# Kernel optimization log

Hardware: AMD Instinct MI355X
Metric: run time of the kernel (lower is better)

## Reference

```python
import jax, jax.numpy as jnp
import numpy as np

# sizes
N, B, NPG = 8192, 8, 1024          # total nodes, graphs, nodes per graph (equal-size graphs)
D, H, DH, L = 256, 8, 32, 2        # hidden, heads, head dim, layers
IN_C, OUT_D, E, DFF = 128, 64, 262144, 512
EPS = 1e-5


def setup_inputs() -> dict:
    key = jax.random.key(0)
    ks = jax.random.split(key, 20)
    p = lambda i, shp: jax.random.normal(ks[i], shp, jnp.float32) * 0.05
    return dict(
        x=jax.random.normal(ks[0], (N, IN_C), jnp.float32),
        edge_index=jax.random.randint(ks[1], (2, E), 0, N),
        batch=jnp.arange(N, dtype=jnp.int32) // NPG,  # sorted, equal-size graphs
        w_in=p(2, (D, IN_C)), b_in=p(3, (D,)),
        sage_wl=p(4, (L, D, D)), sage_bl=p(5, (L, D)), sage_wr=p(6, (L, D, D)),
        attn_iw=p(7, (L, 3 * D, D)), attn_ib=p(8, (L, 3 * D)),
        attn_ow=p(9, (L, D, D)), attn_ob=p(10, (L, D)),
        n1_w=jnp.ones((L, D)), n1_b=jnp.zeros((L, D)),
        n2_w=jnp.ones((L, D)), n2_b=jnp.zeros((L, D)),
        n3_w=jnp.ones((L, D)), n3_b=jnp.zeros((L, D)),
        mlp_w1=p(11, (L, DFF, D)), mlp_b1=p(12, (L, DFF)),
        mlp_w2=p(13, (L, D, DFF)), mlp_b2=p(14, (L, D)),
        bn_w=jnp.ones((L, D)), bn_b=jnp.zeros((L, D)),
        w_out=p(15, (OUT_D, D)), b_out=p(16, (OUT_D,)),
    )


def _bn(h, w, b):
    # BatchNorm1d over nodes (training-mode batch statistics, biased var)
    m = h.mean(0)
    v = jnp.mean((h - m) ** 2, axis=0)
    return (h - m) * jax.lax.rsqrt(v + EPS) * w + b


def _forward(x, edge_index, batch, w_in, b_in, sage_wl, sage_bl, sage_wr,
             attn_iw, attn_ib, attn_ow, attn_ob, n1_w, n1_b, n2_w, n2_b,
             n3_w, n3_b, mlp_w1, mlp_b1, mlp_w2, mlp_b2, bn_w, bn_b, w_out, b_out):
    src, dst = edge_index[0], edge_index[1]
    deg = jax.ops.segment_sum(jnp.ones((E,), jnp.float32), dst, num_segments=N)
    inv_deg = (1.0 / jnp.clip(deg, 1.0))[:, None]
    scale = 1.0 / np.sqrt(DH)

    h = x @ w_in.T + b_in  # in_proj Linear  [N, D]
    for l in range(L):
        # --- GPSConv: local SAGEConv (mean aggr) + residual + norm1 ---
        agg = jax.ops.segment_sum(h[src], dst, num_segments=N) * inv_deg
        loc = agg @ sage_wl[l].T + sage_bl[l] + h @ sage_wr[l].T
        loc = _bn(loc + h, n1_w[l], n1_b[l])
        # --- GPSConv: dense per-graph multi-head self-attention + residual + norm2 ---
        hd = h.reshape(B, NPG, D)  # to_dense_batch (no padding: equal graph sizes)
        qkv = hd @ attn_iw[l].T + attn_ib[l]  # [B, n, 3D]
        q, k, v = jnp.split(qkv, 3, axis=-1)
        sh = lambda t: t.reshape(B, NPG, H, DH).transpose(0, 2, 1, 3)  # [B, H, n, DH]
        a = jax.nn.softmax(jnp.einsum('bhqd,bhkd->bhqk', sh(q) * scale, sh(k)), axis=-1)
        o = jnp.einsum('bhqk,bhkd->bhqd', a, sh(v)).transpose(0, 2, 1, 3).reshape(B, NPG, D)
        o = (o @ attn_ow[l].T + attn_ob[l]).reshape(N, D)
        glob = _bn(o + h, n2_w[l], n2_b[l])
        # --- GPSConv: sum branches, MLP residual, norm3 ---
        out = loc + glob
        out = out + jax.nn.relu(out @ mlp_w1[l].T + mlp_b1[l]) @ mlp_w2[l].T + mlp_b2[l]
        out = _bn(out, n3_w[l], n3_b[l])
        # --- outer GPS: BatchNorm + relu + (dropout=eval) + residual ---
        h = h + jax.nn.relu(_bn(out, bn_w[l], bn_b[l]))
    pooled = h.reshape(B, NPG, D).mean(axis=1)  # global_mean_pool over sorted equal-size graphs
    return pooled @ w_out.T + b_out  # [B, OUT_D]


def reference(x, edge_index, batch, w_in, b_in, sage_wl, sage_bl, sage_wr,
              attn_iw, attn_ib, attn_ow, attn_ob, n1_w, n1_b, n2_w, n2_b,
              n3_w, n3_b, mlp_w1, mlp_b1, mlp_w2, mlp_b2, bn_w, bn_b, w_out, b_out):
    return _forward(x, edge_index, batch, w_in, b_in, sage_wl, sage_bl, sage_wr,
                    attn_iw, attn_ib, attn_ow, attn_ob, n1_w, n1_b, n2_w, n2_b,
                    n3_w, n3_b, mlp_w1, mlp_b1, mlp_w2, mlp_b2, bn_w, bn_b, w_out, b_out)
```

## Files before the change

### kernel.cpp

```cpp
#include <hip/hip_runtime.h>
#include <hip/hip_bf16.h>

#define N_NODES 8192
#define BGRAPH 8
#define NPG 1024
#define DIM 256
#define NH 8
#define DHEAD 32
#define NLAYERS 2
#define INC 128
#define OUTD 64
#define NEDGE 262144
#define DFF 512
#define EPS 1e-5f

typedef __attribute__((ext_vector_type(4))) float f32x4;
typedef __attribute__((ext_vector_type(8))) short s16x8;
typedef __attribute__((ext_vector_type(4))) ushort u16x4;

__device__ __forceinline__ float b2f(ushort u){
  unsigned v = ((unsigned)u) << 16;
  return __builtin_bit_cast(float, v);
}
__device__ __forceinline__ ushort f2b(float f){
  unsigned u = __builtin_bit_cast(unsigned, f);
  u += 0x7fffu + ((u >> 16) & 1u);
  return (ushort)(u >> 16);
}
__device__ __forceinline__ ushort f2b_trunc(float f){
  return (ushort)(__builtin_bit_cast(unsigned, f) >> 16);
}
__device__ __forceinline__ void gload16(const void* g, void* l){
  __builtin_amdgcn_global_load_lds(
    (const __attribute__((address_space(1))) void*)g,
    (__attribute__((address_space(3))) void*)l,
    16, 0, 0);
}

#define CX  1048576
#define CWI (CX+32768)
#define CSW (CWI+262144)
#define CIW (CSW+393216)
#define COW (CIW+131072)
#define CW1 (COW+262144)
#define CW2 (CW1+262144)
#define NCAST (CW2/256)
__global__ void k_setup(const float* __restrict__ x, const float* __restrict__ w_in,
    const float* __restrict__ wl, const float* __restrict__ wr,
    const float* __restrict__ iw, const float* __restrict__ ow,
    const float* __restrict__ w1, const float* __restrict__ w2,
    ushort* __restrict__ dst, const int* __restrict__ edst, int* __restrict__ deg){
  if(blockIdx.x >= NCAST){
    int i = (blockIdx.x - NCAST)*256 + threadIdx.x;
    int stride = 512*256;
    for(; i<NEDGE; i+=stride) atomicAdd(&deg[edst[i]], 1);
    return;
  }
  int i = blockIdx.x*256 + threadIdx.x;
  float val;
  if(i < CX)       val = x[i];
  else if(i < CWI) val = w_in[i-CX];
  else if(i < CSW){
    int j = i - CWI;
    int l = j >> 17, r = (j >> 9) & 255, k = j & 511;
    val = (k < 256) ? wl[(l<<16) + (r<<8) + k] : wr[(l<<16) + (r<<8) + (k-256)];
  }
  else if(i < CIW) val = iw[i-CSW];
  else if(i < COW) val = ow[i-CIW];
  else if(i < CW1) val = w1[i-COW];
  else             val = w2[i-CW1];
  dst[i] = f2b(val);
}

__global__ void k_scan(const int* __restrict__ deg, int* __restrict__ offs,
                       float* __restrict__ inv_deg){
  __shared__ int s[1024];
  int t = threadIdx.x;
  int base = t*8;
  int loc[8]; int acc=0;
  #pragma unroll
  for(int j=0;j<8;j++){
    int dv = deg[base+j];
    inv_deg[base+j] = 1.0f/(float)(dv>0?dv:1);
    loc[j]=acc; acc += dv;
  }
  s[t]=acc;
  __syncthreads();
  for(int d=1; d<1024; d<<=1){
    int v = (t>=d)? s[t-d] : 0;
    __syncthreads();
    if(t>=d) s[t]+=v;
    __syncthreads();
  }
  int pre = (t>0)? s[t-1] : 0;
  #pragma unroll
  for(int j=0;j<8;j++) offs[base+j] = pre + loc[j];
  if(t==1023) offs[N_NODES] = s[1023];
}

#define STAGE_AB(t, buf) do{ \
    int kt_ = (t)*64; \
    _Pragma("unroll") \
    for(int it=0; it<2; ++it){ \
      int c = (wave*2+it)*64 + lane; \
      int row = c >> 3, q = c & 7; \
      int qs = q ^ (row & 7); \
      gload16(A + (size_t)(bm+row)*lda + kt_ + qs*8, (char*)As + (buf)*8192 + (wave*2+it)*1024); \
      gload16(W + (size_t)(bn+row)*K   + kt_ + qs*8, (char*)Bs + (buf)*8192 + (wave*2+it)*1024); \
    } \
  }while(0)

#define MM_COMPUTE(BUFOFF) \
      _Pragma("unroll") \
      for(int kk=0; kk<2; ++kk){ \
        s16x8 af[2], bfr[2]; \
        _Pragma("unroll") \
        for(int mi=0; mi<2; ++mi){ \
          int row = wr*32 + mi*16 + l15; \
          int col = (kk*64 + l4*16) ^ ((row & 7) << 4); \
          af[mi] = *(const s16x8*)((const char*)As + (BUFOFF) + row*128 + col); \
        } \
        _Pragma("unroll") \
        for(int nj=0; nj<2; ++nj){ \
          int row = wc*32 + nj*16 + l15; \
          int col = (kk*64 + l4*16) ^ ((row & 7) << 4); \
          bfr[nj] = *(const s16x8*)((const char*)Bs + (BUFOFF) + row*128 + col); \
        } \
        _Pragma("unroll") \
        for(int mi=0; mi<2; ++mi) \
          _Pragma("unroll") \
          for(int nj=0; nj<2; ++nj) \
            acc[mi][nj] = __builtin_amdgcn_mfma_f32_16x16x32_bf16(af[mi], bfr[nj], acc[mi][nj], 0,0,0); \
      }

#define MM_LOOP \
  f32x4 acc[2][2] = {}; \
  { const int nt = K >> 6; \
    STAGE_AB(0, 0); \
    asm volatile("s_waitcnt vmcnt(0)" ::: "memory"); \
    __builtin_amdgcn_s_barrier(); \
    int cur = 0; \
    for(int t=0; t<nt; ++t){ \
      if(t+1 < nt) STAGE_AB(t+1, cur^1); \
      MM_COMPUTE(cur*8192) \
      asm volatile("s_waitcnt vmcnt(0)" ::: "memory"); \
      __builtin_amdgcn_s_barrier(); \
      cur ^= 1; \
    } \
  }

#define MM_LOOP_SB \
  f32x4 acc[2][2] = {}; \
  { const int nt = K >> 6; \
    for(int t=0; t<nt; ++t){ \
      __syncthreads(); \
      STAGE_AB(t, 0); \
      asm volatile("s_waitcnt vmcnt(0)" ::: "memory"); \
      __builtin_amdgcn_s_barrier(); \
      MM_COMPUTE(0) \
    } \
  }

template<bool RELU, bool RESIDB, bool BIAS, bool WBF, bool STATS>
__global__ __launch_bounds__(256) void k_mm(const ushort* __restrict__ A,
    const ushort* __restrict__ W, const float* __restrict__ bias,
    const ushort* __restrict__ residb, ushort* __restrict__ Cb,
    float* __restrict__ gS, float* __restrict__ gQ,
    int M, int Nc, int K, int lda, int ldcb, int ldrb)
{
  __shared__ ushort As[2*64*64];
  __shared__ ushort Bs[2*64*64];
  __shared__ float sredS[64];
  __shared__ float sredQ[64];
  const int tid = threadIdx.x;
  const int lane = tid & 63, wave = tid >> 6;
  const int l15 = lane & 15, l4 = lane >> 4;
  const int bm = blockIdx.y*64, bn = blockIdx.x*64;
  const int wr = wave >> 1, wc = wave & 1;
  MM_LOOP

  float sloc[2] = {0.f,0.f}, qloc[2] = {0.f,0.f};
  #pragma unroll
  for(int mi=0; mi<2; ++mi){
    #pragma unroll
    for(int nj=0; nj<2; ++nj){
      int col = bn + wc*32 + nj*16 + l15;
      float bv = BIAS ? bias[col] : 0.f;
      #pragma unroll
      for(int r=0; r<4; ++r){
        int row = bm + wr*32 + mi*16 + l4*4 + r;
        float v = acc[mi][nj][r] + bv;
        if(RESIDB) v += b2f(residb[(size_t)row*ldrb + col]);
        if(RELU)   v = fmaxf(v, 0.f);
        if(WBF)    Cb[(size_t)row*ldcb + col] = f2b(v);
        if(STATS){ sloc[nj] += v; qloc[nj] += v*v; }
      }
    }
  }
  if(STATS){
    if(tid < 64){ sredS[tid]=0.f; sredQ[tid]=0.f; }
    __syncthreads();
    int c0 = wc*32 + l15;
    atomicAdd(&sredS[c0],    sloc[0]); atomicAdd(&sredQ[c0],    qloc[0]);
    atomicAdd(&sredS[c0+16], sloc[1]); atomicAdd(&sredQ[c0+16], qloc[1]);
    __syncthreads();
    if(tid < 64){
      atomicAdd(&gS[bn+tid], sredS[tid]);
      atomicAdd(&gQ[bn+tid], sredQ[tid]);
    }
  }
}

__global__ __launch_bounds__(256) void k_fill_inproj(const int* __restrict__ src,
    const int* __restrict__ dst, const int* __restrict__ offs,
    int* __restrict__ cursor, int* __restrict__ csr,
    const ushort* __restrict__ xb, const ushort* __restrict__ w_in_b,
    const float* __restrict__ b_in, ushort* __restrict__ hwb)
{
  __shared__ __align__(16) char smem[16384];
  const int tid = threadIdx.x;
  if(blockIdx.x < 512){
    int i = blockIdx.x*256 + tid;
    for(; i<NEDGE; i+=512*256){
      int d = dst[i];
      int p = atomicAdd(&cursor[d], 1);
      csr[offs[d]+p] = src[i];
    }
  } else {
    int idx = blockIdx.x - 512;
    const int lane = tid & 63, wave = tid >> 6;
    const int l15 = lane & 15, l4 = lane >> 4;
    const int bn = (idx & 3)*64, bm = (idx >> 2)*64;
    const int wr = wave >> 1, wc = wave & 1;
    const ushort* A = xb;
    const ushort* W = w_in_b;
    const int K = INC, lda = INC;
    ushort* As = (ushort*)smem;
    ushort* Bs = As + 4096;
    MM_LOOP_SB
    #pragma unroll
    for(int mi=0; mi<2; ++mi){
      #pragma unroll
      for(int nj=0; nj<2; ++nj){
        int col = bn + wc*32 + nj*16 + l15;
        float bv = b_in[col];
        #pragma unroll
        for(int r=0; r<4; ++r){
          int row = bm + wr*32 + mi*16 + l4*4 + r;
          hwb[(size_t)row*512 + 256 + col] = f2b(acc[mi][nj][r] + bv);
        }
      }
    }
  }
}

__global__ __launch_bounds__(256) void k_agg_qkv(ushort* __restrict__ hwb,
    const int* __restrict__ offs, const int* __restrict__ csr,
    const float* __restrict__ inv_deg, const ushort* __restrict__ iwb,
    const float* __restrict__ attn_ib, ushort* __restrict__ qpack,
    ushort* __restrict__ kpack, ushort* __restrict__ vpack)
{
  __shared__ __align__(16) char smem[16384];
  const int tid = threadIdx.x;
  const int lane = tid & 63, wave = tid >> 6;
  if(blockIdx.x < 2048){
    int n = blockIdx.x*4 + wave;
    int beg = offs[n], end = offs[n+1];
    f32x4 a0 = {0,0,0,0}, a1 = {0,0,0,0}, a2 = {0,0,0,0}, a3 = {0,0,0,0};
    int i = beg;
    for(; i+4<=end; i+=4){
      int j0=csr[i], j1=csr[i+1], j2=csr[i+2], j3=csr[i+3];
      u16x4 v0 = *(const u16x4*)(hwb + (size_t)j0*512 + 256 + lane*4);
      u16x4 v1 = *(const u16x4*)(hwb + (size_t)j1*512 + 256 + lane*4);
      u16x4 v2 = *(const u16x4*)(hwb + (size_t)j2*512 + 256 + lane*4);
      u16x4 v3 = *(const u16x4*)(hwb + (size_t)j3*512 + 256 + lane*4);
      #pragma unroll
      for(int c=0;c<4;c++){ a0[c]+=b2f(v0[c]); a1[c]+=b2f(v1[c]);
                            a2[c]+=b2f(v2[c]); a3[c]+=b2f(v3[c]); }
    }
    for(; i<end; ++i){
      int j0=csr[i];
      u16x4 v0 = *(const u16x4*)(hwb + (size_t)j0*512 + 256 + lane*4);
      #pragma unroll
      for(int c=0;c<4;c++) a0[c]+=b2f(v0[c]);
    }
    float inv = inv_deg[n];
    u16x4 outv;
    #pragma unroll
    for(int c=0;c<4;c++) outv[c] = f2b((a0[c]+a1[c]+a2[c]+a3[c])*inv);
    *(u16x4*)(hwb + (size_t)n*512 + lane*4) = outv;
  } else {
    int idx = blockIdx.x - 2048;
    const int bn = (idx % 12)*64, bm = (idx / 12)*64;
    const int l15 = lane & 15, l4 = lane >> 4;
    const int wr = wave >> 1, wc = wave & 1;
    const ushort* A = hwb + 256;
    const ushort* W = iwb;
    const int K = 256, lda = 512;
    ushort* As = (ushort*)smem;
    ushort* Bs = As + 4096;
    MM_LOOP_SB
    const int bgq = bm >> 10;
    #pragma unroll
    for(int mi=0; mi<2; ++mi){
      #pragma unroll
      for(int nj=0; nj<2; ++nj){
        int col = bn + wc*32 + nj*16 + l15;
        float bv = attn_ib[col];
        int part = col >> 8;
        int hh = (col >> 5) & 7;
        int dd = col & 31;
        ushort* dstp = (part==0 ? qpack : (part==1 ? kpack : vpack))
                     + (size_t)(bgq*8 + hh)*32768 + dd;
        #pragma unroll
        for(int r=0; r<4; ++r){
          int rig = (bm + wr*32 + mi*16 + l4*4 + r) & 1023;
          dstp[rig*32] = f2b(acc[mi][nj][r] + bv);
        }
      }
    }
  }
}

__global__ __launch_bounds__(256) void k_attn_sage(const ushort* __restrict__ qpack,
    const ushort* __restrict__ kpack, const ushort* __restrict__ vpack,
    ushort* __restrict__ attnO, const ushort* __restrict__ hwb,
    const ushort* __restrict__ swb, const float* __restrict__ sage_bl,
    ushort* __restrict__ locB, float* __restrict__ gS, float* __restrict__ gQ)
{
  __shared__ __align__(16) char smem[20992];
  const int tid = threadIdx.x;
  const int lane = tid & 63, wave = tid >> 6;
  const int l15 = lane & 15;
  if(blockIdx.x < 1024){
    ushort* KsB = (ushort*)smem;
    ushort* VtB = (ushort*)smem + 6144;
    const int g = lane >> 4;
    int bid = blockIdx.x;
    int h  = bid & 7;
    int bg = (bid >> 3) & 7;
    int qc = bid >> 6;
    const int bgh = bid & 63;
    const int nb = bg*NPG + qc*64 + wave*16;
    const ushort* qp = qpack + (size_t)bgh*32768;
    const ushort* kp = kpack + (size_t)bgh*32768;
    const ushort* vp = vpack + (size_t)bgh*32768;

    const int rho = tid >> 2, qq = tid & 3;
    const int grp = rho >> 5, r32 = rho & 31;
    const int tt = r32 >> 4, wi = r32 & 15;
    const int jperm = grp*32 + (wi >> 2)*8 + tt*4 + (wi & 3);
    const int qs = qq ^ ((rho >> 1) & 3);

    s16x8 qf = *(const s16x8*)(qp + (qc*64 + wave*16 + l15)*32 + g*8);
    {
      const float scale2 = 0.2550370703637335f;
      #pragma unroll
      for(int i=0;i<8;i++) qf[i] = (short)f2b(b2f((ushort)qf[i]) * scale2);
    }
    f32x4 o0 = {0.f,0.f,0.f,0.f}, o1 = {0.f,0.f,0.f,0.f};
    float mrun = -1e30f, lrun = 0.f;

    gload16(kp + (size_t)jperm*32 + qs*8, (char*)KsB + wave*1024);
    s16x8 vcur = *(const s16x8*)(vp + (size_t)lane*32 + wave*8);

    for(int st=0; st<16; ++st){
      int vb = st & 1;
      int kbuf = st % 3;
      ushort* vtb = VtB + vb*2048;
      #pragma unroll
      for(int i=0;i<8;i++){
        int d = wave*8 + i;
        vtb[d*64 + (lane ^ (i<<3))] = (ushort)vcur[i];
      }
      s16x8 vnext = vcur;
      if(st+1 < 16){
        gload16(kp + (size_t)((st+1)*64 + jperm)*32 + qs*8,
                (char*)(KsB + ((st+1)%3)*2048) + wave*1024);
        vnext = *(const s16x8*)(vp + (size_t)((st+1)*64 + lane)*32 + wave*8);
      }
      asm volatile("s_waitcnt lgkmcnt(0)" ::: "memory");
      __builtin_amdgcn_s_barrier();

      const char* ksb = (const char*)(KsB + kbuf*2048);
      f32x4 sc[4];
      __builtin_amdgcn_s_setprio(1);
      #pragma unroll
      for(int q4=0; q4<4; ++q4){
        int r0 = q4*16 + l15;
        s16x8 kf = *(const s16x8*)(ksb + r0*64 + ((g*16) ^ (((r0>>1)&3)<<4)));
        f32x4 z = {0.f,0.f,0.f,0.f};
        sc[q4] = __builtin_amdgcn_mfma_f32_16x16x32_bf16(kf, qf, z, 0,0,0);
      }
      __builtin_amdgcn_s_setprio(0);

      float smax = -1e30f;
      #pragma unroll
      for(int q4=0; q4<4; ++q4)
        #pragma unroll
        for(int r=0; r<4; ++r) smax = fmaxf(smax, sc[q4][r]);
      smax = fmaxf(smax, __shfl_xor(smax, 16));
      smax = fmaxf(smax, __shfl_xor(smax, 32));

      if(!__all((int)(smax <= mrun + 8.0f))){
        float mnew = fmaxf(mrun, smax);
        float alpha = exp2f(mrun - mnew);
        lrun *= alpha;
        #pragma unroll
        for(int r=0;r<4;r++){
          float ar = __shfl(alpha, (lane & 48) | (g*4 + r), 64);
          o0[r] *= ar; o1[r] *= ar;
        }
        mrun = mnew;
      }

      float p[16];
      float ps = 0.f;
      #pragma unroll
      for(int q4=0; q4<4; ++q4)
        #pragma unroll
        for(int r=0; r<4; ++r){
          float pv = exp2f(sc[q4][r] - mrun);
          p[q4*4+r] = pv; ps += pv;
        }
      ps += __shfl_xor(ps, 16);
      ps += __shfl_xor(ps, 32);
      lrun += ps;

      s16x8 pa0, pa1;
      #pragma unroll
      for(int i=0;i<8;i++){ pa0[i] = (short)f2b_trunc(p[i]); pa1[i] = (short)f2b_trunc(p[8+i]); }

      const char* vtc = (const char*)(VtB + vb*2048);
      int colb0 = g*16, colb1 = 64 + g*16;
      int d0 = l15, d1 = l15 + 16;
      s16x8 v00 = *(const s16x8*)(vtc + d0*128 + (colb0 ^ ((d0&7)<<4)));
      s16x8 v01 = *(const s16x8*)(vtc + d1*128 + (colb0 ^ ((d1&7)<<4)));
      s16x8 v10 = *(const s16x8*)(vtc + d0*128 + (colb1 ^ ((d0&7)<<4)));
      s16x8 v11 = *(const s16x8*)(vtc + d1*128 + (colb1 ^ ((d1&7)<<4)));
      __builtin_amdgcn_s_setprio(1);
      o0 = __builtin_amdgcn_mfma_f32_16x16x32_bf16(pa0, v00, o0, 0,0,0);
      o1 = __builtin_amdgcn_mfma_f32_16x16x32_bf16(pa0, v01, o1, 0,0,0);
      o0 = __builtin_amdgcn_mfma_f32_16x16x32_bf16(pa1, v10, o0, 0,0,0);
      o1 = __builtin_amdgcn_mfma_f32_16x16x32_bf16(pa1, v11, o1, 0,0,0);
      __builtin_amdgcn_s_setprio(0);

      vcur = vnext;
    }
    float inv = 1.0f/lrun;
    #pragma unroll
    for(int r=0;r<4;r++){
      int q2 = g*4 + r;
      float ir = __shfl(inv, (lane & 48) | q2, 64);
      size_t nrow = (size_t)(nb + q2)*DIM + h*32;
      attnO[nrow + l15]      = f2b(o0[r]*ir);
      attnO[nrow + 16 + l15] = f2b(o1[r]*ir);
    }
  } else {
    int idx = blockIdx.x - 1024;
    const int bn = (idx & 3)*64, bm = (idx >> 2)*64;
    const int l4 = lane >> 4;
    const int wr = wave >> 1, wc = wave & 1;
    const ushort* A = hwb;
    const ushort* W = swb;
    const int K = 512, lda = 512;
    ushort* As = (ushort*)smem;
    ushort* Bs = As + 4096;
    float* sredS = (float*)(smem + 16384);
    float* sredQ = sredS + 64;
    MM_LOOP_SB

    float sloc[2] = {0.f,0.f}, qloc[2] = {0.f,0.f};
    #pragma unroll
    for(int mi=0; mi<2; ++mi){
      #pragma unroll
      for(int nj=0; nj<2; ++nj){
        int col = bn + wc*32 + nj*16 + l15;
        float bv = sage_bl[col];
        #pragma unroll
        for(int r=0; r<4; ++r){
          int row = bm + wr*32 + mi*16 + l4*4 + r;
          float v = acc[mi][nj][r] + bv + b2f(hwb[(size_t)row*512 + 256 + col]);
          locB[(size_t)row*DIM + col] = f2b(v);
          sloc[nj] += v; qloc[nj] += v*v;
        }
      }
    }
    if(tid < 64){ sredS[tid]=0.f; sredQ[tid]=0.f; }
    __syncthreads();
    int c0 = wc*32 + l15;
    atomicAdd(&sredS[c0],    sloc[0]); atomicAdd(&sredQ[c0],    qloc[0]);
    atomicAdd(&sredS[c0+16], sloc[1]); atomicAdd(&sredQ[c0+16], qloc[1]);
    __syncthreads();
    if(tid < 64){
      atomicAdd(&gS[bn+tid], sredS[tid]);
      atomicAdd(&gQ[bn+tid], sredQ[tid]);
    }
  }
}

__global__ __launch_bounds__(256) void k_apply12(const ushort* __restrict__ locB,
    const ushort* __restrict__ globB, const float* __restrict__ slot,
    const float* __restrict__ n1w, const float* __restrict__ n1b,
    const float* __restrict__ n2w, const float* __restrict__ n2b,
    ushort* __restrict__ combB){
  int t = blockIdx.x*256 + threadIdx.x;
  int base = t*4;
  int d0 = base & 255;
  u16x4 lv = *(const u16x4*)(locB + base);
  u16x4 gv = *(const u16x4*)(globB + base);
  f32x4 s1 = *(const f32x4*)(slot + d0);
  f32x4 q1 = *(const f32x4*)(slot + 256 + d0);
  f32x4 s2 = *(const f32x4*)(slot + 512 + d0);
  f32x4 q2 = *(const f32x4*)(slot + 768 + d0);
  f32x4 w1v = *(const f32x4*)(n1w + d0);
  f32x4 b1v = *(const f32x4*)(n1b + d0);
  f32x4 w2v = *(const f32x4*)(n2w + d0);
  f32x4 b2v = *(const f32x4*)(n2b + d0);
  const float invn = 1.0f/N_NODES;
  u16x4 outv;
  #pragma unroll
  for(int c=0;c<4;c++){
    float m1 = s1[c]*invn, v1 = q1[c]*invn - m1*m1;
    float m2 = s2[c]*invn, v2 = q2[c]*invn - m2*m2;
    float y1 = (b2f(lv[c])-m1)*rsqrtf(v1+EPS)*w1v[c] + b1v[c];
    float y2 = (b2f(gv[c])-m2)*rsqrtf(v2+EPS)*w2v[c] + b2v[c];
    outv[c] = f2b(y1 + y2);
  }
  *(u16x4*)(combB + base) = outv;
}

__global__ __launch_bounds__(256) void k_apply3o(const ushort* __restrict__ xB,
    const float* __restrict__ slot, const float* __restrict__ n3w,
    const float* __restrict__ bw, const float* __restrict__ bb,
    ushort* __restrict__ hwbR){
  int t = blockIdx.x*256 + threadIdx.x;
  int base = t*4;
  int d0 = base & 255;
  int row = base >> 8;
  u16x4 xv = *(const u16x4*)(xB + base);
  u16x4 hv = *(const u16x4*)(hwbR + (size_t)row*512 + d0);
  f32x4 s3 = *(const f32x4*)(slot + 1024 + d0);
  f32x4 q3 = *(const f32x4*)(slot + 1280 + d0);
  f32x4 wv3 = *(const f32x4*)(n3w + d0);
  f32x4 bwv = *(const f32x4*)(bw + d0);
  f32x4 bbv = *(const f32x4*)(bb + d0);
  const float invn = 1.0f/N_NODES;
  u16x4 outv;
  #pragma unroll
  for(int c=0;c<4;c++){
    float m = s3[c]*invn, var = q3[c]*invn - m*m;
    float rs = rsqrtf(var+EPS);
    float gch = rs*wv3[c];
    float rso = rsqrtf(gch*gch*var + EPS);
    float yo = (b2f(xv[c])-m)*gch*rso*bwv[c] + bbv[c];
    outv[c] = f2b(b2f(hv[c]) + fmaxf(yo, 0.f));
  }
  *(u16x4*)(hwbR + (size_t)row*512 + d0) = outv;
}

__global__ void k_pool(const ushort* __restrict__ hwbR, float* __restrict__ pooled){
  int b = blockIdx.x, c = blockIdx.y, d = threadIdx.x;
  int r0 = c*64;
  float s=0.f;
  for(int i=0;i<64;i++) s += b2f(hwbR[(size_t)(b*NPG + r0 + i)*512 + d]);
  atomicAdd(&pooled[b*DIM+d], s*(1.0f/NPG));
}
__global__ void k_out(const float* __restrict__ pooled, const float* __restrict__ w_out,
                      const float* __restrict__ b_out, float* __restrict__ out){
  int t = threadIdx.x;
  if(t >= BGRAPH*OUTD) return;
  int b = t/OUTD, oc = t%OUTD;
  float s = b_out[oc];
  for(int k=0;k<DIM;k++) s += pooled[b*DIM+k]*w_out[oc*DIM+k];
  out[t] = s;
}

extern "C" void kernel_launch(void* const* d_in, const int* in_sizes, int n_in,
                              void* d_out, int out_size, void* d_ws, size_t ws_size,
                              hipStream_t stream) {
  const float* x       = (const float*)d_in[0];
  const int*   edge    = (const int*)d_in[1];
  const float* w_in    = (const float*)d_in[3];
  const float* b_in    = (const float*)d_in[4];
  const float* sage_wl = (const float*)d_in[5];
  const float* sage_bl = (const float*)d_in[6];
  const float* sage_wr = (const float*)d_in[7];
  const float* attn_iw = (const float*)d_in[8];
  const float* attn_ib = (const float*)d_in[9];
  const float* attn_ow = (const float*)d_in[10];
  const float* attn_ob = (const float*)d_in[11];
  const float* n1_w = (const float*)d_in[12];
  const float* n1_b = (const float*)d_in[13];
  const float* n2_w = (const float*)d_in[14];
  const float* n2_b = (const float*)d_in[15];
  const float* n3_w = (const float*)d_in[16];
  const float* n3_b = (const float*)d_in[17];
  const float* mlp_w1 = (const float*)d_in[18];
  const float* mlp_b1 = (const float*)d_in[19];
  const float* mlp_w2 = (const float*)d_in[20];
  const float* mlp_b2 = (const float*)d_in[21];
  const float* bn_w = (const float*)d_in[22];
  const float* bn_b = (const float*)d_in[23];
  const float* w_out = (const float*)d_in[24];
  const float* b_out = (const float*)d_in[25];

  const size_t ND = (size_t)N_NODES*DIM;
  ushort* wsb   = (ushort*)d_ws;
  ushort* locB  = wsb;
  ushort* globB = wsb + ND;
  ushort* hwb   = wsb + 2*ND;
  ushort* qpack = wsb + 4*ND;
  ushort* kpack = wsb + 5*ND;
  ushort* vpack = wsb + 6*ND;
  ushort* attnOb= wsb + 7*ND;
  ushort* combb = wsb + 8*ND;
  ushort* hidb  = wsb + 9*ND;
  ushort* castb = wsb + 11*ND;
  ushort* xb     = castb;
  ushort* w_in_b = castb + CX;
  ushort* sageWb = castb + CWI;
  ushort* iw_b   = castb + CSW;
  ushort* ow_b   = castb + CIW;
  ushort* w1_b   = castb + COW;
  ushort* w2_b   = castb + CW1;
  float* mf      = (float*)(castb + CW2);
  float* inv_deg = mf;
  float* bnslots = mf + 8192;
  float* pooled  = bnslots + 3072;
  int* deg    = (int*)(pooled + 2048);
  int* cursor = deg + N_NODES;
  int* offs   = cursor + N_NODES;
  int* csr    = offs + N_NODES + 8;

  const int* esrc = edge;
  const int* edst = edge + NEDGE;

  hipMemsetAsync(bnslots, 0, (3072+2048)*sizeof(float) + 2*N_NODES*sizeof(int), stream);

  k_setup<<<NCAST+512,256,0,stream>>>(x, w_in, sage_wl, sage_wr, attn_iw,
      attn_ow, mlp_w1, mlp_w2, castb, edst, deg);
  k_scan<<<1,1024,0,stream>>>(deg, offs, inv_deg);

  k_fill_inproj<<<1024,256,0,stream>>>(esrc, edst, offs, cursor, csr,
      xb, w_in_b, b_in, hwb);

  for(int l=0; l<NLAYERS; ++l){
    const ushort* swb = sageWb + (size_t)l*131072;
    const ushort* iwb = iw_b + (size_t)l*196608;
    const ushort* owb = ow_b + (size_t)l*65536;
    const ushort* w1b = w1_b + (size_t)l*131072;
    const ushort* w2b = w2_b + (size_t)l*131072;
    float* slot = bnslots + (size_t)l*1536;

    k_agg_qkv<<<3584,256,0,stream>>>(hwb, offs, csr, inv_deg, iwb,
        attn_ib + l*3*DIM, qpack, kpack, vpack);

    k_attn_sage<<<1536,256,0,stream>>>(qpack, kpack, vpack, attnOb, hwb, swb,
        sage_bl + l*DIM, locB, slot, slot+256);

    k_mm<false,true,true,true,true><<<dim3(4,128),256,0,stream>>>(
        attnOb, owb, attn_ob + l*DIM, hwb+256, globB, slot+512, slot+768,
        N_NODES, DIM, DIM, DIM, DIM, 512);

    k_apply12<<<2048,256,0,stream>>>(locB, globB, slot,
        n1_w + l*DIM, n1_b + l*DIM, n2_w + l*DIM, n2_b + l*DIM, combb);

    k_mm<true,false,true,true,false><<<dim3(8,128),256,0,stream>>>(
        combb, w1b, mlp_b1 + l*DFF, nullptr, hidb, nullptr, nullptr,
        N_NODES, DFF, DIM, DIM, 512, 256);

    k_mm<false,true,true,true,true><<<dim3(4,128),256,0,stream>>>(
        hidb, w2b, mlp_b2 + l*DIM, combb, globB, slot+1024, slot+1280,
        N_NODES, DIM, 512, 512, DIM, 256);

    k_apply3o<<<2048,256,0,stream>>>(globB, slot, n3_w + l*DIM,
        bn_w + l*DIM, bn_b + l*DIM, hwb+256);
  }

  k_pool<<<dim3(BGRAPH, NPG/64),256,0,stream>>>(hwb+256, pooled);
  k_out<<<1,512,0,stream>>>(pooled, w_out, b_out, (float*)d_out);
}
```

Measured before the change: 259.1 us.

## Process two query tiles per wave in attention to reuse K/V loads

```diff
diff --git a/kernel.cpp b/kernel.cpp
--- a/kernel.cpp
+++ b/kernel.cpp
@@ -332,7 +332,7 @@
   const int tid = threadIdx.x;
   const int lane = tid & 63, wave = tid >> 6;
   const int l15 = lane & 15;
-  if(blockIdx.x < 1024){
+  if(blockIdx.x < 512){
     ushort* KsB = (ushort*)smem;
     ushort* VtB = (ushort*)smem + 6144;
     const int g = lane >> 4;
@@ -341,7 +341,7 @@
     int bg = (bid >> 3) & 7;
     int qc = bid >> 6;
     const int bgh = bid & 63;
-    const int nb = bg*NPG + qc*64 + wave*16;
+    const int nb = bg*NPG + qc*128 + wave*32;
     const ushort* qp = qpack + (size_t)bgh*32768;
     const ushort* kp = kpack + (size_t)bgh*32768;
     const ushort* vp = vpack + (size_t)bgh*32768;
@@ -352,14 +352,21 @@
     const int jperm = grp*32 + (wi >> 2)*8 + tt*4 + (wi & 3);
     const int qs = qq ^ ((rho >> 1) & 3);
 
-    s16x8 qf = *(const s16x8*)(qp + (qc*64 + wave*16 + l15)*32 + g*8);
+    const int qrow = qc*128 + wave*32 + l15;
+    s16x8 qf0 = *(const s16x8*)(qp + (size_t)qrow*32 + g*8);
+    s16x8 qf1 = *(const s16x8*)(qp + (size_t)(qrow+16)*32 + g*8);
     {
       const float scale2 = 0.2550370703637335f;
       #pragma unroll
-      for(int i=0;i<8;i++) qf[i] = (short)f2b(b2f((ushort)qf[i]) * scale2);
+      for(int i=0;i<8;i++){
+        qf0[i] = (short)f2b(b2f((ushort)qf0[i]) * scale2);
+        qf1[i] = (short)f2b(b2f((ushort)qf1[i]) * scale2);
+      }
     }
     f32x4 o0 = {0.f,0.f,0.f,0.f}, o1 = {0.f,0.f,0.f,0.f};
-    float mrun = -1e30f, lrun = 0.f;
+    f32x4 o2 = {0.f,0.f,0.f,0.f}, o3 = {0.f,0.f,0.f,0.f};
+    float mrun0 = -1e30f, lrun0 = 0.f;
+    float mrun1 = -1e30f, lrun1 = 0.f;
 
     gload16(kp + (size_t)jperm*32 + qs*8, (char*)KsB + wave*1024);
     s16x8 vcur = *(const s16x8*)(vp + (size_t)lane*32 + wave*8);
@@ -383,14 +390,15 @@
       __builtin_amdgcn_s_barrier();
 
       const char* ksb = (const char*)(KsB + kbuf*2048);
-      f32x4 sc[4];
+      f32x4 sc0[4], sc1[4];
       __builtin_amdgcn_s_setprio(1);
       #pragma unroll
       for(int q4=0; q4<4; ++q4){
         int r0 = q4*16 + l15;
         s16x8 kf = *(const s16x8*)(ksb + r0*64 + ((g*16) ^ (((r0>>1)&3)<<4)));
         f32x4 z = {0.f,0.f,0.f,0.f};
-        sc[q4] = __builtin_amdgcn_mfma_f32_16x16x32_bf16(kf, qf, z, 0,0,0);
+        sc0[q4] = __builtin_amdgcn_mfma_f32_16x16x32_bf16(kf, qf0, z, 0,0,0);
+        sc1[q4] = __builtin_amdgcn_mfma_f32_16x16x32_bf16(kf, qf1, z, 0,0,0);
       }
       __builtin_amdgcn_s_setprio(0);
 
@@ -398,38 +406,72 @@
       #pragma unroll
       for(int q4=0; q4<4; ++q4)
         #pragma unroll
-        for(int r=0; r<4; ++r) smax = fmaxf(smax, sc[q4][r]);
+        for(int r=0; r<4; ++r) smax = fmaxf(smax, sc0[q4][r]);
       smax = fmaxf(smax, __shfl_xor(smax, 16));
       smax = fmaxf(smax, __shfl_xor(smax, 32));
-
-      if(!__all((int)(smax <= mrun + 8.0f))){
-        float mnew = fmaxf(mrun, smax);
-        float alpha = exp2f(mrun - mnew);
-        lrun *= alpha;
+      if(!__all((int)(smax <= mrun0 + 8.0f))){
+        float mnew = fmaxf(mrun0, smax);
+        float alpha = exp2f(mrun0 - mnew);
+        lrun0 *= alpha;
         #pragma unroll
         for(int r=0;r<4;r++){
           float ar = __shfl(alpha, (lane & 48) | (g*4 + r), 64);
           o0[r] *= ar; o1[r] *= ar;
         }
-        mrun = mnew;
-      }
-
-      float p[16];
-      float ps = 0.f;
+        mrun0 = mnew;
+      }
+      s16x8 pa00, pa01;
+      {
+        float ps = 0.f;
+        float p[16];
+        #pragma unroll
+        for(int q4=0; q4<4; ++q4)
+          #pragma unroll
+          for(int r=0; r<4; ++r){
+            float pv = exp2f(sc0[q4][r] - mrun0);
+            p[q4*4+r] = pv; ps += pv;
+          }
+        ps += __shfl_xor(ps, 16);
+        ps += __shfl_xor(ps, 32);
+        lrun0 += ps;
+        #pragma unroll
+        for(int i=0;i<8;i++){ pa00[i] = (short)f2b_trunc(p[i]); pa01[i] = (short)f2b_trunc(p[8+i]); }
+      }
+      float smax1 = -1e30f;
       #pragma unroll
       for(int q4=0; q4<4; ++q4)
         #pragma unroll
-        for(int r=0; r<4; ++r){
-          float pv = exp2f(sc[q4][r] - mrun);
-          p[q4*4+r] = pv; ps += pv;
+        for(int r=0; r<4; ++r) smax1 = fmaxf(smax1, sc1[q4][r]);
+      smax1 = fmaxf(smax1, __shfl_xor(smax1, 16));
+      smax1 = fmaxf(smax1, __shfl_xor(smax1, 32));
+      if(!__all((int)(smax1 <= mrun1 + 8.0f))){
+        float mnew = fmaxf(mrun1, smax1);
+        float alpha = exp2f(mrun1 - mnew);
+        lrun1 *= alpha;
+        #pragma unroll
+        for(int r=0;r<4;r++){
+          float ar = __shfl(alpha, (lane & 48) | (g*4 + r), 64);
+          o2[r] *= ar; o3[r] *= ar;
         }
-      ps += __shfl_xor(ps, 16);
-      ps += __shfl_xor(ps, 32);
-      lrun += ps;
-
-      s16x8 pa0, pa1;
-      #pragma unroll
-      for(int i=0;i<8;i++){ pa0[i] = (short)f2b_trunc(p[i]); pa1[i] = (short)f2b_trunc(p[8+i]); }
+        mrun1 = mnew;
+      }
+      s16x8 pa10, pa11;
+      {
+        float ps = 0.f;
+        float p[16];
+        #pragma unroll
+        for(int q4=0; q4<4; ++q4)
+          #pragma unroll
+          for(int r=0; r<4; ++r){
+            float pv = exp2f(sc1[q4][r] - mrun1);
+            p[q4*4+r] = pv; ps += pv;
+          }
+        ps += __shfl_xor(ps, 16);
+        ps += __shfl_xor(ps, 32);
+        lrun1 += ps;
+        #pragma unroll
+        for(int i=0;i<8;i++){ pa10[i] = (short)f2b_trunc(p[i]); pa11[i] = (short)f2b_trunc(p[8+i]); }
+      }
 
       const char* vtc = (const char*)(VtB + vb*2048);
       int colb0 = g*16, colb1 = 64 + g*16;
@@ -439,25 +481,34 @@
       s16x8 v10 = *(const s16x8*)(vtc + d0*128 + (colb1 ^ ((d0&7)<<4)));
       s16x8 v11 = *(const s16x8*)(vtc + d1*128 + (colb1 ^ ((d1&7)<<4)));
       __builtin_amdgcn_s_setprio(1);
-      o0 = __builtin_amdgcn_mfma_f32_16x16x32_bf16(pa0, v00, o0, 0,0,0);
-      o1 = __builtin_amdgcn_mfma_f32_16x16x32_bf16(pa0, v01, o1, 0,0,0);
-      o0 = __builtin_amdgcn_mfma_f32_16x16x32_bf16(pa1, v10, o0, 0,0,0);
-      o1 = __builtin_amdgcn_mfma_f32_16x16x32_bf16(pa1, v11, o1, 0,0,0);
+      o0 = __builtin_amdgcn_mfma_f32_16x16x32_bf16(pa00, v00, o0, 0,0,0);
+      o1 = __builtin_amdgcn_mfma_f32_16x16x32_bf16(pa00, v01, o1, 0,0,0);
+      o0 = __builtin_amdgcn_mfma_f32_16x16x32_bf16(pa01, v10, o0, 0,0,0);
+      o1 = __builtin_amdgcn_mfma_f32_16x16x32_bf16(pa01, v11, o1, 0,0,0);
+      o2 = __builtin_amdgcn_mfma_f32_16x16x32_bf16(pa10, v00, o2, 0,0,0);
+      o3 = __builtin_amdgcn_mfma_f32_16x16x32_bf16(pa10, v01, o3, 0,0,0);
+      o2 = __builtin_amdgcn_mfma_f32_16x16x32_bf16(pa11, v10, o2, 0,0,0);
+      o3 = __builtin_amdgcn_mfma_f32_16x16x32_bf16(pa11, v11, o3, 0,0,0);
       __builtin_amdgcn_s_setprio(0);
 
       vcur = vnext;
     }
-    float inv = 1.0f/lrun;
+    float inv0 = 1.0f/lrun0;
+    float inv1 = 1.0f/lrun1;
     #pragma unroll
     for(int r=0;r<4;r++){
       int q2 = g*4 + r;
-      float ir = __shfl(inv, (lane & 48) | q2, 64);
-      size_t nrow = (size_t)(nb + q2)*DIM + h*32;
-      attnO[nrow + l15]      = f2b(o0[r]*ir);
-      attnO[nrow + 16 + l15] = f2b(o1[r]*ir);
+      float ir0 = __shfl(inv0, (lane & 48) | q2, 64);
+      float ir1 = __shfl(inv1, (lane & 48) | q2, 64);
+      size_t nrow0 = (size_t)(nb + q2)*DIM + h*32;
+      size_t nrow1 = (size_t)(nb + 16 + q2)*DIM + h*32;
+      attnO[nrow0 + l15]      = f2b(o0[r]*ir0);
+      attnO[nrow0 + 16 + l15] = f2b(o1[r]*ir0);
+      attnO[nrow1 + l15]      = f2b(o2[r]*ir1);
+      attnO[nrow1 + 16 + l15] = f2b(o3[r]*ir1);
     }
   } else {
-    int idx = blockIdx.x - 1024;
+    int idx = blockIdx.x - 512;
     const int bn = (idx & 3)*64, bm = (idx >> 2)*64;
     const int l4 = lane >> 4;
     const int wr = wave >> 1, wc = wave & 1;
@@ -656,7 +707,7 @@
     k_agg_qkv<<<3584,256,0,stream>>>(hwb, offs, csr, inv_deg, iwb,
         attn_ib + l*3*DIM, qpack, kpack, vpack);
 
-    k_attn_sage<<<1536,256,0,stream>>>(qpack, kpack, vpack, attnOb, hwb, swb,
+    k_attn_sage<<<1024,256,0,stream>>>(qpack, kpack, vpack, attnOb, hwb, swb,
         sage_bl + l*DIM, locB, slot, slot+256);
 
     k_mm<false,true,true,true,true><<<dim3(4,128),256,0,stream>>>(
```

Result: slower. 266.6 us (+2.9%).
